# Kernel tuning notes

Hardware: AMD Instinct MI355X
Metric: run time of the kernel (lower is better)

## Reference

```python
import jax, jax.numpy as jnp
import numpy as np

V, BLOCK, L, H, E = 1000, 1024, 8, 16, 1024
D = E // H
HID = 4 * E
B, S = 4, 1024
NEG = -1e9


def setup_inputs() -> dict:
    key = jax.random.key(0)
    ks = jax.random.split(key, 10)
    s = 0.02
    rn = lambda k, shp: jax.random.normal(k, shp, jnp.float32) * s
    return dict(
        idx=jax.random.randint(ks[0], (B, S), 0, V),
        wte=rn(ks[1], (V, E)),
        wpe=rn(ks[2], (BLOCK, E)),
        ln1_w=jnp.ones((L, E), jnp.float32), ln1_b=jnp.zeros((L, E), jnp.float32),
        qkv_w=rn(ks[3], (L, E, 3 * E)), qkv_b=jnp.zeros((L, 3 * E), jnp.float32),
        out_w=rn(ks[4], (L, E, E)), out_b=jnp.zeros((L, E), jnp.float32),
        ln2_w=jnp.ones((L, E), jnp.float32), ln2_b=jnp.zeros((L, E), jnp.float32),
        fc1_w=rn(ks[5], (L, E, HID)), fc1_b=jnp.zeros((L, HID), jnp.float32),
        fc2_w=rn(ks[6], (L, HID, E)), fc2_b=jnp.zeros((L, E), jnp.float32),
        lnf_w=jnp.ones((E,), jnp.float32), lnf_b=jnp.zeros((E,), jnp.float32),
        head_w=rn(ks[7], (E, V)), head_b=jnp.zeros((V,), jnp.float32),
    )


def _ln(x, w, b):
    m = x.mean(-1, keepdims=True)
    v = x.var(-1, keepdims=True)
    return (x - m) / jnp.sqrt(v + 1e-5) * w + b


def _block(x, p):
    (ln1_w, ln1_b, qkv_w, qkv_b, out_w, out_b,
     ln2_w, ln2_b, fc1_w, fc1_b, fc2_w, fc2_b) = p
    b, s, _ = x.shape
    # --- causal self-attention ---
    h = _ln(x, ln1_w, ln1_b)
    qkv = h @ qkv_w + qkv_b                           # [b, s, 3E]
    q, k, v = jnp.split(qkv, 3, axis=-1)
    q = q.reshape(b, s, H, D)
    k = k.reshape(b, s, H, D)
    v = v.reshape(b, s, H, D)
    att = jnp.einsum('bqhd,bkhd->bhqk', q, k) / np.sqrt(D).astype(np.float32)
    mask = jnp.tril(jnp.ones((s, s), bool))
    att = jnp.where(mask, att, NEG)
    att = jax.nn.softmax(att, axis=-1)
    y = jnp.einsum('bhqk,bkhd->bqhd', att, v).reshape(b, s, E)
    x = x + (y @ out_w + out_b)
    # --- MLP ---
    h = _ln(x, ln2_w, ln2_b)
    h = jax.nn.gelu(h @ fc1_w + fc1_b, approximate=False)
    x = x + (h @ fc2_w + fc2_b)
    return x


def reference(idx, wte, wpe, ln1_w, ln1_b, qkv_w, qkv_b, out_w, out_b,
              ln2_w, ln2_b, fc1_w, fc1_b, fc2_w, fc2_b, lnf_w, lnf_b,
              head_w, head_b):
    s = idx.shape[1]
    x = wte[idx] + wpe[:s]                            # [B, S, E]
    layer_params = (ln1_w, ln1_b, qkv_w, qkv_b, out_w, out_b,
                    ln2_w, ln2_b, fc1_w, fc1_b, fc2_w, fc2_b)
    def step(x, p):
        return _block(x, p), None
    x, _ = jax.lax.scan(step, x, layer_params)
    x = _ln(x, lnf_w, lnf_b)
    logits = x @ head_w + head_b                      # [B, S, V]
    return logits
```

## Files before the change

### kernel.cpp

```cpp
#include <hip/hip_runtime.h>
#include <math.h>


typedef unsigned short u16;
typedef unsigned int u32;
typedef __attribute__((ext_vector_type(4))) float f32x4;
typedef __attribute__((ext_vector_type(8))) __bf16 bf16x8;
typedef __attribute__((ext_vector_type(8))) u16 u16x8;
typedef __attribute__((ext_vector_type(4))) u16 u16x4;

#define E 1024
#define HID 4096
#define NH 16
#define HD 64
#define SEQ 1024
#define NB 4
#define NL 8
#define MTOK 4096
#define VOC 1000

#define VMCNT(n) asm volatile("s_waitcnt vmcnt(" #n ")" ::: "memory")

__device__ __forceinline__ u16 f2bf(float f){
  u32 u = __float_as_uint(f);
  u32 r = (u + 0x7fffu + ((u >> 16) & 1u)) >> 16;
  return (u16)r;
}
__device__ __forceinline__ float bf2f(u16 b){
  return __uint_as_float((u32)b << 16);
}
__device__ __forceinline__ bf16x8 ld_bf8(const u16* p){
  return *reinterpret_cast<const bf16x8*>(p);
}
__device__ __forceinline__ bf16x8 as_bf(u16x8 v){
  return __builtin_bit_cast(bf16x8, v);
}

__device__ __forceinline__ void gload16(const void* g, void* l){
  __builtin_amdgcn_global_load_lds(
      (const __attribute__((address_space(1))) void*)g,
      (__attribute__((address_space(3))) void*)l, 16, 0, 0);
}

__global__ __launch_bounds__(256) void embed_kernel(
    const int* __restrict__ idx, const float* __restrict__ wte,
    const float* __restrict__ wpe, float* __restrict__ x)
{
  int tok = blockIdx.x, tid = threadIdx.x;
  int id = idx[tok];
  int s = tok & (SEQ - 1);
  f32x4 a = *reinterpret_cast<const f32x4*>(&wte[(size_t)id * E + tid * 4]);
  f32x4 p = *reinterpret_cast<const f32x4*>(&wpe[(size_t)s * E + tid * 4]);
  f32x4 r = a + p;
  *reinterpret_cast<f32x4*>(&x[(size_t)tok * E + tid * 4]) = r;
}

__global__ __launch_bounds__(256) void ln_kernel(
    const float* __restrict__ x, const float* __restrict__ w,
    const float* __restrict__ b, u16* __restrict__ h)
{
  int row = blockIdx.x, tid = threadIdx.x;
  const float* xr = x + (size_t)row * E;
  f32x4 v = *reinterpret_cast<const f32x4*>(xr + tid * 4);
  float s = v[0] + v[1] + v[2] + v[3];
  float q = v[0]*v[0] + v[1]*v[1] + v[2]*v[2] + v[3]*v[3];
  #pragma unroll
  for (int mm = 1; mm < 64; mm <<= 1){
    s += __shfl_xor(s, mm);
    q += __shfl_xor(q, mm);
  }
  __shared__ float red[8];
  int wv = tid >> 6;
  if ((tid & 63) == 0){ red[wv] = s; red[4 + wv] = q; }
  __syncthreads();
  s = red[0] + red[1] + red[2] + red[3];
  q = red[4] + red[5] + red[6] + red[7];
  float mean = s * (1.0f / E);
  float var = q * (1.0f / E) - mean * mean;
  float rstd = rsqrtf(var + 1e-5f);
  f32x4 wv4 = *reinterpret_cast<const f32x4*>(w + tid * 4);
  f32x4 bv4 = *reinterpret_cast<const f32x4*>(b + tid * 4);
  u16 o0 = f2bf((v[0] - mean) * rstd * wv4[0] + bv4[0]);
  u16 o1 = f2bf((v[1] - mean) * rstd * wv4[1] + bv4[1]);
  u16 o2 = f2bf((v[2] - mean) * rstd * wv4[2] + bv4[2]);
  u16 o3 = f2bf((v[3] - mean) * rstd * wv4[3] + bv4[3]);
  u16* hp = &h[(size_t)row * E + tid * 4];
  hp[0] = o0; hp[1] = o1; hp[2] = o2; hp[3] = o3;
}

__global__ __launch_bounds__(256) void wconv4_kernel(
    const float* __restrict__ qw, const float* __restrict__ ow,
    const float* __restrict__ f1, const float* __restrict__ f2,
    u16* __restrict__ dq, u16* __restrict__ dо_unused, u16* __restrict__ d1,
    u16* __restrict__ d2, u16* __restrict__ dw_out)
{
  const int bid = blockIdx.x, tid = threadIdx.x;
  const float* W; u16* Wt; int K, Nsrc, nx, base;
  if (bid < 768)      { W = qw; Wt = dq;     K = 1024; Nsrc = 3072; nx = 48; base = 0; }
  else if (bid < 1024){ W = ow; Wt = dw_out; K = 1024; Nsrc = 1024; nx = 16; base = 768; }
  else if (bid < 2048){ W = f1; Wt = d1;     K = 1024; Nsrc = 4096; nx = 64; base = 1024; }
  else                { W = f2; Wt = d2;     K = 4096; Nsrc = 1024; nx = 16; base = 2048; }
  const int t = bid - base;
  const int n0 = (t % nx) * 64, k0 = (t / nx) * 64;

  __shared__ float T[64][65];
  const int c = (tid & 15) * 4, rbase = tid >> 4;
  #pragma unroll
  for (int p = 0; p < 4; p++){
    int r = rbase + p * 16;
    f32x4 v = *reinterpret_cast<const f32x4*>(&W[(size_t)(k0 + r) * Nsrc + n0 + c]);
    T[r][c] = v[0]; T[r][c+1] = v[1]; T[r][c+2] = v[2]; T[r][c+3] = v[3];
  }
  __syncthreads();
  const int nr = tid >> 2, ks = (tid & 3) * 16;
  u16x8 o0, o1;
  #pragma unroll
  for (int i = 0; i < 8; i++){
    o0[i] = f2bf(T[ks + i][nr]);
    o1[i] = f2bf(T[ks + 8 + i][nr]);
  }
  u16* dst = &Wt[(size_t)(n0 + nr) * K + k0 + ks];
  *reinterpret_cast<u16x8*>(dst) = o0;
  *reinterpret_cast<u16x8*>(dst + 8) = o1;
}

__global__ __launch_bounds__(256) void wconv_kernel(
    const float* __restrict__ W, u16* __restrict__ Wt,
    int K, int Nsrc, int N)
{
  __shared__ float T[64][65];
  const int tid = threadIdx.x;
  const int n0 = blockIdx.x * 64, k0 = blockIdx.y * 64;
  const int c = (tid & 15) * 4, rbase = tid >> 4;
  #pragma unroll
  for (int p = 0; p < 4; p++){
    int r = rbase + p * 16;
    #pragma unroll
    for (int j = 0; j < 4; j++){
      int n = n0 + c + j;
      T[r][c + j] = (n < Nsrc) ? W[(size_t)(k0 + r) * Nsrc + n] : 0.0f;
    }
  }
  __syncthreads();
  const int nr = tid >> 2, ks = (tid & 3) * 16;
  u16x8 o0, o1;
  #pragma unroll
  for (int i = 0; i < 8; i++){
    o0[i] = f2bf(T[ks + i][nr]);
    o1[i] = f2bf(T[ks + 8 + i][nr]);
  }
  u16* dst = &Wt[(size_t)(n0 + nr) * K + k0 + ks];
  *reinterpret_cast<u16x8*>(dst) = o0;
  *reinterpret_cast<u16x8*>(dst + 8) = o1;
}

enum { EPI_BF16 = 0, EPI_GELU = 1, EPI_RESID = 2, EPI_OUT = 3 };

template<int EPI, int NW, int NWX, int FM, int FN, int NS, int MINW>
__global__ __launch_bounds__(NW * 64, MINW) void gemm2_kernel(
    const u16* __restrict__ A, const u16* __restrict__ Wt,
    const float* __restrict__ bias, void* __restrict__ outp,
    float* __restrict__ xres, int M, int N, int K)
{
  constexpr int BM = FM * 16 * (NW / NWX);
  constexpr int BN = FN * 16 * NWX;
  constexpr int SLOT = (BM + BN) * 32;
  constexpr int RPW = (BM + BN) / 16 / NW;
  extern __shared__ u16 lds[];

  const int tid = threadIdx.x;
  const int lane = tid & 63, w = tid >> 6;
  const int l15 = lane & 15, g = lane >> 4;
  const int wr = w / NWX, wc = w % NWX;
  const int wrbase = wr * FM * 16, wcbase = wc * FN * 16;

  const int nwgx = gridDim.x;
  const int bid = blockIdx.y * nwgx + blockIdx.x;
  const int cpx = (nwgx * gridDim.y) >> 3;
  const int swz = (bid & 7) * cpx + (bid >> 3);
  const int bm = (swz / nwgx) * BM, bn = (swz % nwgx) * BN;

  const u16* Abase = A + (size_t)bm * K;
  const u16* Bbase = Wt + (size_t)bn * K;

  f32x4 acc[FM][FN];
  #pragma unroll
  for (int i = 0; i < FM; i++)
    #pragma unroll
    for (int j = 0; j < FN; j++)
      acc[i][j] = f32x4{0.f, 0.f, 0.f, 0.f};

  const int lr = lane >> 2, ps = lane & 3;
  const int ss = ps ^ ((lane >> 4) & 3);
  auto STAGE = [&](int s, int cc){
    const int k0 = cc * 32;
    u16* As = lds + s * SLOT;
    u16* Bs = As + BM * 32;
    #pragma unroll
    for (int j = 0; j < RPW; j++){
      int base = (w * RPW + j) * 16;
      if (base < BM){
        gload16(&Abase[(size_t)(base + lr) * K + k0 + ss * 8], As + base * 32);
      } else {
        int rb = base - BM;
        gload16(&Bbase[(size_t)(rb + lr) * K + k0 + ss * 8], Bs + rb * 32);
      }
    }
  };

  const int nt = K >> 5;
  STAGE(0, 0);
  STAGE(1, 1);
  if constexpr (NS == 4) STAGE(2, 2);
  int sl = 0;
  for (int c = 0; c < nt; c++){
    const int rem = nt - 1 - c;
    if constexpr (NS == 4){
      if (rem >= 2)      { VMCNT(8); }
      else if (rem == 1) { VMCNT(4); }
      else               { VMCNT(0); }
    } else {
      if (rem >= 1)      { VMCNT(4); }
      else               { VMCNT(0); }
    }
    __builtin_amdgcn_sched_barrier(0);
    __builtin_amdgcn_s_barrier();
    __builtin_amdgcn_sched_barrier(0);

    const u16* As = lds + sl * SLOT;
    const u16* Bs = As + BM * 32;
    bf16x8 af[FM], bf[FN];
    const int rsw = (g ^ (l15 >> 2)) * 8;
    #pragma unroll
    for (int mf = 0; mf < FM; mf++)
      af[mf] = ld_bf8(&As[(wrbase + mf * 16 + l15) * 32 + rsw]);
    #pragma unroll
    for (int nf = 0; nf < FN; nf++)
      bf[nf] = ld_bf8(&Bs[(wcbase + nf * 16 + l15) * 32 + rsw]);
    __builtin_amdgcn_s_setprio(1);
    #pragma unroll
    for (int mf = 0; mf < FM; mf++)
      #pragma unroll
      for (int nf = 0; nf < FN; nf++)
        acc[mf][nf] = __builtin_amdgcn_mfma_f32_16x16x32_bf16(
            af[mf], bf[nf], acc[mf][nf], 0, 0, 0);
    __builtin_amdgcn_s_setprio(0);

    if (c + NS - 1 < nt){
      int s2 = sl + NS - 1; if (s2 >= NS) s2 -= NS;
      STAGE(s2, c + NS - 1);
    }
    sl++; if (sl >= NS) sl -= NS;
  }

  #pragma unroll
  for (int mf = 0; mf < FM; mf++){
    #pragma unroll
    for (int nf = 0; nf < FN; nf++){
      int col = bn + wcbase + nf * 16 + l15;
      float bv = bias[col];
      #pragma unroll
      for (int r = 0; r < 4; r++){
        int row = bm + wrbase + mf * 16 + g * 4 + r;
        float v = acc[mf][nf][r] + bv;
        if constexpr (EPI == EPI_BF16){
          ((u16*)outp)[(size_t)row * N + col] = f2bf(v);
        } else if constexpr (EPI == EPI_GELU){
          ((u16*)outp)[(size_t)row * N + col] =
              f2bf(0.5f * v * (1.0f + erff(v * 0.70710678118654752f)));
        } else if constexpr (EPI == EPI_RESID){
          xres[(size_t)row * N + col] += v;
        } else {
          if (col < VOC)
            ((float*)outp)[(size_t)row * VOC + col] = v;
        }
      }
    }
  }
}

__global__ __launch_bounds__(256) void attn_kernel(
    const u16* __restrict__ qkv, u16* __restrict__ y)
{
  __shared__ u16 Kl[64 * 64];
  __shared__ u16 Vt[64 * 72];
  __shared__ u16 Pl[4 * 16 * 72];
  const int pr = blockIdx.x, hh = blockIdx.y, b = blockIdx.z;
  const int tid = threadIdx.x;
  const int lane = tid & 63, w = tid >> 6;
  const int l15 = lane & 15, g = lane >> 4;
  const size_t tokbase = (size_t)b * SEQ;
  const int qstart[2] = { pr * 64, (15 - pr) * 64 };

  int qbase[2], dt[2];
  u16x8 q0[2], q1[2];
  f32x4 o[2][4];
  float m[2][4], llp[2][4];
  #pragma unroll
  for (int st = 0; st < 2; st++){
    qbase[st] = qstart[st] + w * 16;
    dt[st] = qbase[st] >> 6;
    const u16* qp = &qkv[(tokbase + qbase[st] + l15) * (3 * E) + hh * HD];
    u16x8 ra = *reinterpret_cast<const u16x8*>(&qp[g * 8]);
    u16x8 rb = *reinterpret_cast<const u16x8*>(&qp[32 + g * 8]);
    #pragma unroll
    for (int j = 0; j < 8; j++){
      q0[st][j] = f2bf(bf2f(ra[j]) * 0.125f);
      q1[st][j] = f2bf(bf2f(rb[j]) * 0.125f);
    }
    #pragma unroll
    for (int dc = 0; dc < 4; dc++) o[st][dc] = f32x4{0.f, 0.f, 0.f, 0.f};
    #pragma unroll
    for (int r = 0; r < 4; r++){ m[st][r] = -1e30f; llp[st][r] = 0.f; }
  }

  u16* Pw = &Pl[w * 16 * 72];
  const int T = 16 - pr;

  for (int t = 0; t < T; t++){
    const int k0 = t * 64;
    __syncthreads();
    #pragma unroll
    for (int j = 0; j < 2; j++){
      int row = w * 16 + j * 8 + (lane >> 3);
      int sl = lane & 7;
      const u16* src = &qkv[(tokbase + k0 + row) * (3 * E) + E + hh * HD
                            + ((sl ^ (row & 7)) * 8)];
      gload16(src, &Kl[w * 1024 + j * 512]);
    }
    {
      int d0 = (tid & 15) * 4;
      int s  = tid >> 4;
      #pragma unroll
      for (int mh = 0; mh < 2; mh++){
        int kA = s + 32 * mh;
        const u16* vpA = &qkv[(tokbase + k0 + kA) * (3 * E) + 2 * E + hh * HD + d0];
        const u16* vpB = vpA + 16 * (3 * E);
        u16x4 va = *reinterpret_cast<const u16x4*>(vpA);
        u16x4 vb = *reinterpret_cast<const u16x4*>(vpB);
        #pragma unroll
        for (int i = 0; i < 4; i++)
          *reinterpret_cast<u32*>(&Vt[(d0 + i) * 72 + 4 * s + 2 * mh]) =
              (u32)va[i] | ((u32)vb[i] << 16);
      }
    }
    __syncthreads();

    #pragma unroll
    for (int st = 0; st < 2; st++){
      if (t > dt[st]) continue;
      const bool diag = (t == dt[st]);
      f32x4 s[4];
      #pragma unroll
      for (int kg = 0; kg < 4; kg++){
        int key = kg * 16 + l15;
        const u16* kb = &Kl[key * 64];
        bf16x8 k0f = ld_bf8(&kb[(g ^ (key & 7)) * 8]);
        bf16x8 k1f = ld_bf8(&kb[((4 + g) ^ (key & 7)) * 8]);
        f32x4 z = f32x4{0.f, 0.f, 0.f, 0.f};
        z = __builtin_amdgcn_mfma_f32_16x16x32_bf16(as_bf(q0[st]), k0f, z, 0, 0, 0);
        z = __builtin_amdgcn_mfma_f32_16x16x32_bf16(as_bf(q1[st]), k1f, z, 0, 0, 0);
        s[kg] = z;
      }
      if (diag){
        #pragma unroll
        for (int kg = 0; kg < 4; kg++){
          int key = k0 + kg * 16 + l15;
          #pragma unroll
          for (int r = 0; r < 4; r++){
            int q = qbase[st] + g * 4 + r;
            s[kg][r] = (key <= q) ? s[kg][r] : -1e9f;
          }
        }
      }
      float lmax[4];
      bool need = false;
      #pragma unroll
      for (int r = 0; r < 4; r++){
        lmax[r] = fmaxf(fmaxf(s[0][r], s[1][r]), fmaxf(s[2][r], s[3][r]));
        need = need || (lmax[r] > m[st][r] + 8.0f);
      }
      if (__any(need)){
        #pragma unroll
        for (int r = 0; r < 4; r++){
          float x = lmax[r];
          x = fmaxf(x, __shfl_xor(x, 1));
          x = fmaxf(x, __shfl_xor(x, 2));
          x = fmaxf(x, __shfl_xor(x, 4));
          x = fmaxf(x, __shfl_xor(x, 8));
          float mn = fmaxf(m[st][r], x);
          float al = __expf(m[st][r] - mn);
          m[st][r] = mn;
          llp[st][r] *= al;
          #pragma unroll
          for (int dc = 0; dc < 4; dc++) o[st][dc][r] *= al;
        }
      }
      #pragma unroll
      for (int r = 0; r < 4; r++){
        float p0 = __expf(s[0][r] - m[st][r]);
        float p1 = __expf(s[1][r] - m[st][r]);
        float p2 = __expf(s[2][r] - m[st][r]);
        float p3 = __expf(s[3][r] - m[st][r]);
        llp[st][r] += (p0 + p1) + (p2 + p3);
        u16x4 pp = { f2bf(p0), f2bf(p1), f2bf(p2), f2bf(p3) };
        *reinterpret_cast<u16x4*>(&Pw[(g * 4 + r) * 72 + 4 * l15]) = pp;
      }
      bf16x8 pa0 = ld_bf8(&Pw[l15 * 72 + g * 8]);
      bf16x8 pa1 = ld_bf8(&Pw[l15 * 72 + 32 + g * 8]);
      #pragma unroll
      for (int dc = 0; dc < 4; dc++){
        bf16x8 v0 = ld_bf8(&Vt[(dc * 16 + l15) * 72 + g * 8]);
        bf16x8 v1 = ld_bf8(&Vt[(dc * 16 + l15) * 72 + 32 + g * 8]);
        o[st][dc] = __builtin_amdgcn_mfma_f32_16x16x32_bf16(pa0, v0, o[st][dc], 0, 0, 0);
        o[st][dc] = __builtin_amdgcn_mfma_f32_16x16x32_bf16(pa1, v1, o[st][dc], 0, 0, 0);
      }
    }
  }

  #pragma unroll
  for (int st = 0; st < 2; st++){
    #pragma unroll
    for (int r = 0; r < 4; r++){
      float rs = llp[st][r];
      rs += __shfl_xor(rs, 1);
      rs += __shfl_xor(rs, 2);
      rs += __shfl_xor(rs, 4);
      rs += __shfl_xor(rs, 8);
      float inv = 1.0f / rs;
      int row = qbase[st] + g * 4 + r;
      #pragma unroll
      for (int dc = 0; dc < 4; dc++){
        int col = hh * HD + dc * 16 + l15;
        y[(tokbase + row) * E + col] = f2bf(o[st][dc][r] * inv);
      }
    }
  }
}

__global__ __launch_bounds__(256) void biaspad_kernel(
    const float* __restrict__ hb, float* __restrict__ bpad)
{
  int i = blockIdx.x * 256 + threadIdx.x;
  if (i < 1024) bpad[i] = (i < VOC) ? hb[i] : 0.0f;
}

extern "C" void kernel_launch(void* const* d_in, const int* in_sizes, int n_in,
                              void* d_out, int out_size, void* d_ws, size_t ws_size,
                              hipStream_t stream)
{
  const int*   idx    = (const int*)  d_in[0];
  const float* wte    = (const float*)d_in[1];
  const float* wpe    = (const float*)d_in[2];
  const float* ln1_w  = (const float*)d_in[3];
  const float* ln1_b  = (const float*)d_in[4];
  const float* qkv_w  = (const float*)d_in[5];
  const float* qkv_b  = (const float*)d_in[6];
  const float* out_w  = (const float*)d_in[7];
  const float* out_b  = (const float*)d_in[8];
  const float* ln2_w  = (const float*)d_in[9];
  const float* ln2_b  = (const float*)d_in[10];
  const float* fc1_w  = (const float*)d_in[11];
  const float* fc1_b  = (const float*)d_in[12];
  const float* fc2_w  = (const float*)d_in[13];
  const float* fc2_b  = (const float*)d_in[14];
  const float* lnf_w  = (const float*)d_in[15];
  const float* lnf_b  = (const float*)d_in[16];
  const float* head_w = (const float*)d_in[17];
  const float* head_b = (const float*)d_in[18];

  char* ws = (char*)d_ws;
  float* x    = (float*)(ws + 0);
  u16*   h    = (u16*)  (ws + 16777216);
  u16*   qkvb = (u16*)  (ws + 25165824);
  u16*   y    = (u16*)  (ws + 50331648);
  u16*   g    = (u16*)  (ws + 58720256);
  u16*   wq   = (u16*)  (ws + 92274688);
  u16*   wo   = (u16*)  (ws + 98566144);
  u16*   w1   = (u16*)  (ws + 100663296);
  u16*   w2   = (u16*)  (ws + 109051904);
  u16*   wh   = (u16*)  (ws + 117440512);
  float* hbp  = (float*)(ws + 119537664);

  constexpr int LDS_BIG = 4 * (512 * 32) * 2;
  constexpr int LDS_SML = 3 * (256 * 32) * 2;
  hipFuncSetAttribute((const void*)gemm2_kernel<EPI_BF16, 8, 4, 8, 4, 4, 2>,
                      hipFuncAttributeMaxDynamicSharedMemorySize, LDS_BIG);
  hipFuncSetAttribute((const void*)gemm2_kernel<EPI_GELU, 8, 4, 8, 4, 4, 2>,
                      hipFuncAttributeMaxDynamicSharedMemorySize, LDS_BIG);

  embed_kernel<<<MTOK, 256, 0, stream>>>(idx, wte, wpe, x);
  biaspad_kernel<<<4, 256, 0, stream>>>(head_b, hbp);

  for (int l = 0; l < NL; l++){
    ln_kernel<<<MTOK, 256, 0, stream>>>(x, ln1_w + l * E, ln1_b + l * E, h);
    wconv4_kernel<<<3072, 256, 0, stream>>>(
        qkv_w + (size_t)l * E * 3 * E, out_w + (size_t)l * E * E,
        fc1_w + (size_t)l * E * HID, fc2_w + (size_t)l * HID * E,
        wq, nullptr, w1, w2, wo);
    gemm2_kernel<EPI_BF16, 8, 4, 8, 4, 4, 2><<<dim3(12, 16), 512, LDS_BIG, stream>>>(
        h, wq, qkv_b + (size_t)l * 3 * E, qkvb, nullptr, MTOK, 3 * E, E);
    attn_kernel<<<dim3(8, NH, NB), 256, 0, stream>>>(qkvb, y);
    gemm2_kernel<EPI_RESID, 4, 2, 4, 4, 3, 3><<<dim3(8, 32), 256, LDS_SML, stream>>>(
        y, wo, out_b + (size_t)l * E, nullptr, x, MTOK, E, E);
    ln_kernel<<<MTOK, 256, 0, stream>>>(x, ln2_w + l * E, ln2_b + l * E, h);
    gemm2_kernel<EPI_GELU, 8, 4, 8, 4, 4, 2><<<dim3(16, 16), 512, LDS_BIG, stream>>>(
        h, w1, fc1_b + (size_t)l * HID, g, nullptr, MTOK, HID, E);
    gemm2_kernel<EPI_RESID, 4, 2, 4, 4, 3, 3><<<dim3(8, 32), 256, LDS_SML, stream>>>(
        g, w2, fc2_b + (size_t)l * E, nullptr, x, MTOK, E, HID);
  }
  ln_kernel<<<MTOK, 256, 0, stream>>>(x, lnf_w, lnf_b, h);
  wconv_kernel<<<dim3(16, 16), 256, 0, stream>>>(head_w, wh, E, VOC, E);
  gemm2_kernel<EPI_OUT, 4, 2, 4, 4, 3, 3><<<dim3(8, 32), 256, LDS_SML, stream>>>(
      h, wh, hbp, (float*)d_out, nullptr, MTOK, E, E);
}
```

Baseline: 1.977 ms.

## Restructure GEMM pipeline to one barrier per K-step with 4-stage buffers everywhere

Moves the vmcnt wait and workgroup barrier from the top of each K iteration to after the LDS fragment reads, with a prologue wait before the loop. This lets the next tile's global loads overlap the current MFMA work and keeps each barrier separating reads from the slot being overwritten. The small GEMMs (out-proj, fc2, head) now use a 4-stage ring instead of 3, which raises their LDS to 64KB and lowers their min-waves launch bound from 3 to 2. That may reduce occupancy for those kernels in exchange for deeper prefetch.

```diff
diff --git a/kernel.cpp b/kernel.cpp
--- a/kernel.cpp
+++ b/kernel.cpp
@@ -91,7 +91,7 @@
 __global__ __launch_bounds__(256) void wconv4_kernel(
     const float* __restrict__ qw, const float* __restrict__ ow,
     const float* __restrict__ f1, const float* __restrict__ f2,
-    u16* __restrict__ dq, u16* __restrict__ dо_unused, u16* __restrict__ d1,
+    u16* __restrict__ dq, u16* __restrict__ d_unused, u16* __restrict__ d1,
     u16* __restrict__ d2, u16* __restrict__ dw_out)
 {
   const int bid = blockIdx.x, tid = threadIdx.x;
@@ -156,7 +156,7 @@
 
 enum { EPI_BF16 = 0, EPI_GELU = 1, EPI_RESID = 2, EPI_OUT = 3 };
 
-template<int EPI, int NW, int NWX, int FM, int FN, int NS, int MINW>
+template<int EPI, int NW, int NWX, int FM, int FN, int MINW>
 __global__ __launch_bounds__(NW * 64, MINW) void gemm2_kernel(
     const u16* __restrict__ A, const u16* __restrict__ Wt,
     const float* __restrict__ bias, void* __restrict__ outp,
@@ -166,6 +166,7 @@
   constexpr int BN = FN * 16 * NWX;
   constexpr int SLOT = (BM + BN) * 32;
   constexpr int RPW = (BM + BN) / 16 / NW;
+  constexpr int NS = 4;
   extern __shared__ u16 lds[];
 
   const int tid = threadIdx.x;
@@ -209,24 +210,14 @@
   };
 
   const int nt = K >> 5;
-  STAGE(0, 0);
-  STAGE(1, 1);
-  if constexpr (NS == 4) STAGE(2, 2);
+  STAGE(0, 0); STAGE(1, 1); STAGE(2, 2);
+  VMCNT(4);
+  __builtin_amdgcn_sched_barrier(0);
+  __builtin_amdgcn_s_barrier();
+  __builtin_amdgcn_sched_barrier(0);
+
   int sl = 0;
   for (int c = 0; c < nt; c++){
-    const int rem = nt - 1 - c;
-    if constexpr (NS == 4){
-      if (rem >= 2)      { VMCNT(8); }
-      else if (rem == 1) { VMCNT(4); }
-      else               { VMCNT(0); }
-    } else {
-      if (rem >= 1)      { VMCNT(4); }
-      else               { VMCNT(0); }
-    }
-    __builtin_amdgcn_sched_barrier(0);
-    __builtin_amdgcn_s_barrier();
-    __builtin_amdgcn_sched_barrier(0);
-
     const u16* As = lds + sl * SLOT;
     const u16* Bs = As + BM * 32;
     bf16x8 af[FM], bf[FN];
@@ -237,6 +228,11 @@
     #pragma unroll
     for (int nf = 0; nf < FN; nf++)
       bf[nf] = ld_bf8(&Bs[(wcbase + nf * 16 + l15) * 32 + rsw]);
+    __builtin_amdgcn_sched_barrier(0);
+    if (c + 2 <= nt - 1) { VMCNT(4); } else { VMCNT(0); }
+    __builtin_amdgcn_sched_barrier(0);
+    __builtin_amdgcn_s_barrier();
+    __builtin_amdgcn_sched_barrier(0);
     __builtin_amdgcn_s_setprio(1);
     #pragma unroll
     for (int mf = 0; mf < FM; mf++)
@@ -245,10 +241,9 @@
         acc[mf][nf] = __builtin_amdgcn_mfma_f32_16x16x32_bf16(
             af[mf], bf[nf], acc[mf][nf], 0, 0, 0);
     __builtin_amdgcn_s_setprio(0);
-
-    if (c + NS - 1 < nt){
-      int s2 = sl + NS - 1; if (s2 >= NS) s2 -= NS;
-      STAGE(s2, c + NS - 1);
+    if (c + 3 < nt){
+      int s2 = sl + 3; if (s2 >= NS) s2 -= NS;
+      STAGE(s2, c + 3);
     }
     sl++; if (sl >= NS) sl -= NS;
   }
@@ -483,11 +478,15 @@
   float* hbp  = (float*)(ws + 119537664);
 
   constexpr int LDS_BIG = 4 * (512 * 32) * 2;
-  constexpr int LDS_SML = 3 * (256 * 32) * 2;
-  hipFuncSetAttribute((const void*)gemm2_kernel<EPI_BF16, 8, 4, 8, 4, 4, 2>,
+  constexpr int LDS_SML = 4 * (256 * 32) * 2;
+  hipFuncSetAttribute((const void*)gemm2_kernel<EPI_BF16, 8, 4, 8, 4, 2>,
                       hipFuncAttributeMaxDynamicSharedMemorySize, LDS_BIG);
-  hipFuncSetAttribute((const void*)gemm2_kernel<EPI_GELU, 8, 4, 8, 4, 4, 2>,
+  hipFuncSetAttribute((const void*)gemm2_kernel<EPI_GELU, 8, 4, 8, 4, 2>,
                       hipFuncAttributeMaxDynamicSharedMemorySize, LDS_BIG);
+  hipFuncSetAttribute((const void*)gemm2_kernel<EPI_RESID, 4, 2, 4, 4, 2>,
+                      hipFuncAttributeMaxDynamicSharedMemorySize, LDS_SML);
+  hipFuncSetAttribute((const void*)gemm2_kernel<EPI_OUT, 4, 2, 4, 4, 2>,
+                      hipFuncAttributeMaxDynamicSharedMemorySize, LDS_SML);
 
   embed_kernel<<<MTOK, 256, 0, stream>>>(idx, wte, wpe, x);
   biaspad_kernel<<<4, 256, 0, stream>>>(head_b, hbp);
@@ -498,19 +497,19 @@
         qkv_w + (size_t)l * E * 3 * E, out_w + (size_t)l * E * E,
         fc1_w + (size_t)l * E * HID, fc2_w + (size_t)l * HID * E,
         wq, nullptr, w1, w2, wo);
-    gemm2_kernel<EPI_BF16, 8, 4, 8, 4, 4, 2><<<dim3(12, 16), 512, LDS_BIG, stream>>>(
+    gemm2_kernel<EPI_BF16, 8, 4, 8, 4, 2><<<dim3(12, 16), 512, LDS_BIG, stream>>>(
         h, wq, qkv_b + (size_t)l * 3 * E, qkvb, nullptr, MTOK, 3 * E, E);
     attn_kernel<<<dim3(8, NH, NB), 256, 0, stream>>>(qkvb, y);
-    gemm2_kernel<EPI_RESID, 4, 2, 4, 4, 3, 3><<<dim3(8, 32), 256, LDS_SML, stream>>>(
+    gemm2_kernel<EPI_RESID, 4, 2, 4, 4, 2><<<dim3(8, 32), 256, LDS_SML, stream>>>(
         y, wo, out_b + (size_t)l * E, nullptr, x, MTOK, E, E);
     ln_kernel<<<MTOK, 256, 0, stream>>>(x, ln2_w + l * E, ln2_b + l * E, h);
-    gemm2_kernel<EPI_GELU, 8, 4, 8, 4, 4, 2><<<dim3(16, 16), 512, LDS_BIG, stream>>>(
+    gemm2_kernel<EPI_GELU, 8, 4, 8, 4, 2><<<dim3(16, 16), 512, LDS_BIG, stream>>>(
         h, w1, fc1_b + (size_t)l * HID, g, nullptr, MTOK, HID, E);
-    gemm2_kernel<EPI_RESID, 4, 2, 4, 4, 3, 3><<<dim3(8, 32), 256, LDS_SML, stream>>>(
+    gemm2_kernel<EPI_RESID, 4, 2, 4, 4, 2><<<dim3(8, 32), 256, LDS_SML, stream>>>(
         g, w2, fc2_b + (size_t)l * E, nullptr, x, MTOK, E, HID);
   }
   ln_kernel<<<MTOK, 256, 0, stream>>>(x, lnf_w, lnf_b, h);
   wconv_kernel<<<dim3(16, 16), 256, 0, stream>>>(head_w, wh, E, VOC, E);
-  gemm2_kernel<EPI_OUT, 4, 2, 4, 4, 3, 3><<<dim3(8, 32), 256, LDS_SML, stream>>>(
+  gemm2_kernel<EPI_OUT, 4, 2, 4, 4, 2><<<dim3(8, 32), 256, LDS_SML, stream>>>(
       h, wh, hbp, (float*)d_out, nullptr, MTOK, E, E);
 }
```

Result: faster. 1.897 ms (-4.0%).
